# Optimization experiments

Hardware: AMD Instinct MI355X
Metric: run time of the kernel (lower is better)

The kernel has to match this reference:

```python
import jax, jax.numpy as jnp
import numpy as np

EMBED_DIM = 1024
N1 = 4096
N2 = 4096


def setup_inputs() -> dict:
    key = jax.random.key(0)
    ks = jax.random.split(key, 14)
    s = 1.0 / np.sqrt(EMBED_DIM)
    def lin(k):
        kw, kb = jax.random.split(k)
        W = jax.random.uniform(kw, (EMBED_DIM, EMBED_DIM), jnp.float32, -s, s)
        b = jax.random.uniform(kb, (EMBED_DIM,), jnp.float32, -s, s)
        return W, b
    Wq1, bq1 = lin(ks[0]); Wk1, bk1 = lin(ks[1]); Wv1, bv1 = lin(ks[2])
    Wq2, bq2 = lin(ks[3]); Wk2, bk2 = lin(ks[4]); Wv2, bv2 = lin(ks[5])
    x1 = jax.random.normal(ks[6], (N1, EMBED_DIM), jnp.float32)
    x2 = jax.random.normal(ks[7], (N2, EMBED_DIM), jnp.float32)
    return {
        "input_tensor1": x1, "input_tensor2": x2,
        "Wq1": Wq1, "bq1": bq1, "Wk1": Wk1, "bk1": bk1, "Wv1": Wv1, "bv1": bv1,
        "Wq2": Wq2, "bq2": bq2, "Wk2": Wk2, "bk2": bk2, "Wv2": Wv2, "bv2": bv2,
    }


def reference(input_tensor1, input_tensor2,
              Wq1, bq1, Wk1, bk1, Wv1, bv1,
              Wq2, bq2, Wk2, bk2, Wv2, bv2):
    scale = 1.0 / jnp.sqrt(jnp.asarray(EMBED_DIM, input_tensor1.dtype))
    # torch Linear: y = x @ W.T + b
    q1 = input_tensor1 @ Wq1.T + bq1   # [N1, D]
    k1 = input_tensor1 @ Wk1.T + bk1
    v1 = input_tensor1 @ Wv1.T + bv1
    q2 = input_tensor2 @ Wq2.T + bq2   # [N2, D]
    k2 = input_tensor2 @ Wk2.T + bk2
    v2 = input_tensor2 @ Wv2.T + bv2
    # stream-2 queries attend over stream-1 keys/values
    scores1 = (q2 @ k1.T) * scale                  # [N2, N1]
    probs1 = jax.nn.softmax(scores1, axis=-1)      # dropout p=0 -> identity
    context1 = probs1 @ v1                         # [N2, D]
    # stream-1 queries attend over stream-2 keys/values
    scores2 = (q1 @ k2.T) * scale                  # [N1, N2]
    probs2 = jax.nn.softmax(scores2, axis=-1)
    context2 = probs2 @ v2                         # [N1, D]
    return (context1, context2)
```

## Files before the change

kernel.cpp:

```cpp
#include <hip/hip_runtime.h>
#include <hip/hip_bf16.h>
#include <cstdint>
#include <cstddef>

#define DEVINL __device__ __forceinline__

typedef __attribute__((ext_vector_type(4))) float   f32x4;
typedef __bf16 bf16x8 __attribute__((ext_vector_type(8)));
typedef __attribute__((ext_vector_type(4))) short   short4v;
typedef __attribute__((ext_vector_type(4))) float   float4v;

static constexpr int BM = 128, BN = 128, BK = 32;
static constexpr int DIM = 1024;
static constexpr int NTOK = 4096;

DEVINL unsigned short f2bf(float f) {
  unsigned u = __float_as_uint(f);
  u += 0x7FFF + ((u >> 16) & 1);
  return (unsigned short)(u >> 16);
}
DEVINL float bf2f(unsigned short s) {
  return __uint_as_float(((unsigned)s) << 16);
}

DEVINL void gll16(const void* g, void* l) {
  __builtin_amdgcn_global_load_lds(
      (const __attribute__((address_space(1))) void*)g,
      (__attribute__((address_space(3))) void*)l, 16, 0, 0);
}

DEVINL void core256(const unsigned short* __restrict__ A, int lda,
                    const unsigned short* __restrict__ B, int ldb,
                    int K, int brow, int bcol, f32x4 acc[8][4])
{
  __shared__ unsigned short lds[65536];
  const int t = threadIdx.x;
  const int w = t >> 6, l = t & 63;
  const int wr = w >> 2, wc = w & 3;
  const int srow = l >> 3;
  const int scol = ((l & 7) ^ srow) << 3;
  const int l15 = l & 15;
  const int cs0 = (((l >> 4) << 3)      ^ ((l & 7) << 3));
  const int cs1 = ((32 + ((l >> 4) << 3)) ^ ((l & 7) << 3));

  const unsigned short* aL = A + (size_t)(brow * 256 + srow) * lda + scol;
  const unsigned short* bL = B + (size_t)(bcol * 256 + srow) * ldb + scol;

#pragma unroll
  for (int m = 0; m < 8; ++m)
#pragma unroll
    for (int n = 0; n < 4; ++n) {
      f32x4 z = {0.f, 0.f, 0.f, 0.f};
      acc[m][n] = z;
    }

#define STA_(Sbase, h, r, kt)                                                  \
  gll16(aL + (size_t)((r)*128 + (h)*64 + (w << 3)) * lda + (size_t)(kt)*64,    \
        (Sbase) + ((r)*128 + (h)*64 + (w << 3)) * 64)
#define STB_(Sbase, h, r, kt)                                                  \
  { const int g16_ = w + (r)*8;                                                \
    const int r0_ = (g16_ >> 2)*64 + (h)*32 + (g16_ & 3)*8;                    \
    gll16(bL + (size_t)r0_ * ldb + (size_t)(kt)*64, (Sbase) + r0_ * 64); }
#define LDA_(Abase, mh)                                                        \
  _Pragma("unroll")                                                            \
  for (int m4 = 0; m4 < 4; ++m4) {                                             \
    const unsigned short* p_ = (Abase) + (wr*128 + (mh)*64 + m4*16 + l15)*64;  \
    af[m4][0] = *(const bf16x8*)(p_ + cs0);                                    \
    af[m4][1] = *(const bf16x8*)(p_ + cs1);                                    \
  }
#define LDB_(Bbase, nh)                                                        \
  _Pragma("unroll")                                                            \
  for (int n2 = 0; n2 < 2; ++n2) {                                             \
    const unsigned short* p_ = (Bbase) + (wc*64 + (nh)*32 + n2*16 + l15)*64;   \
    bfr[n2][0] = *(const bf16x8*)(p_ + cs0);                                   \
    bfr[n2][1] = *(const bf16x8*)(p_ + cs1);                                   \
  }
#define MF_(mh, nh)                                                            \
  __builtin_amdgcn_s_setprio(1);                                               \
  _Pragma("unroll")                                                            \
  for (int m4 = 0; m4 < 4; ++m4)                                               \
  _Pragma("unroll")                                                            \
  for (int n2 = 0; n2 < 2; ++n2) {                                             \
    f32x4 c_ = acc[(mh)*4 + m4][(nh)*2 + n2];                                  \
    c_ = __builtin_amdgcn_mfma_f32_16x16x32_bf16(af[m4][0], bfr[n2][0], c_, 0,0,0); \
    c_ = __builtin_amdgcn_mfma_f32_16x16x32_bf16(af[m4][1], bfr[n2][1], c_, 0,0,0); \
    acc[(mh)*4 + m4][(nh)*2 + n2] = c_;                                        \
  }                                                                            \
  __builtin_amdgcn_s_setprio(0);
#define VMW4() asm volatile("s_waitcnt vmcnt(4)" ::: "memory")
#define VMW2() asm volatile("s_waitcnt vmcnt(2)" ::: "memory")
#define VMW0() asm volatile("s_waitcnt vmcnt(0)" ::: "memory")
#define LGW()  do { asm volatile("s_waitcnt lgkmcnt(0)" ::: "memory");         \
                    __builtin_amdgcn_sched_barrier(0); } while (0)
#define BARR() do { __builtin_amdgcn_s_barrier();                              \
                    asm volatile("" ::: "memory"); } while (0)

  {
    unsigned short* S0 = lds;
    STA_(S0, 0, 0, 0); STA_(S0, 0, 1, 0);
    STB_(S0 + 16384, 0, 0, 0); STB_(S0 + 16384, 0, 1, 0);
    STA_(S0, 1, 0, 0); STA_(S0, 1, 1, 0);
    STB_(S0 + 16384, 1, 0, 0); STB_(S0 + 16384, 1, 1, 0);
  }

  bf16x8 af[4][2], bfr[2][2];
  const int NT = K >> 6;
  for (int kt = 0; kt < NT - 1; ++kt) {
    const unsigned short* Ab = lds + (kt & 1) * 32768;
    const unsigned short* Bb = Ab + 16384;
    unsigned short* Sa = lds + ((kt & 1) ^ 1) * 32768;
    unsigned short* Sb = Sa + 16384;

    VMW4(); BARR();
    STA_(Sa, 0, 0, kt + 1); STA_(Sa, 0, 1, kt + 1);
    LDA_(Ab, 0); LDB_(Bb, 0);
    LGW(); MF_(0, 0);

    VMW4(); BARR();
    STB_(Sb, 0, 0, kt + 1); STB_(Sb, 0, 1, kt + 1);
    LDA_(Ab, 1);
    LGW(); MF_(1, 0);

    VMW4(); BARR();
    STA_(Sa, 1, 0, kt + 1); STA_(Sa, 1, 1, kt + 1);
    LDB_(Bb, 1);
    LGW(); MF_(1, 1);

    STB_(Sb, 1, 0, kt + 1); STB_(Sb, 1, 1, kt + 1);
    LDA_(Ab, 0);
    LGW(); MF_(0, 1);
  }

  {
    const int kt = NT - 1;
    const unsigned short* Ab = lds + (kt & 1) * 32768;
    const unsigned short* Bb = Ab + 16384;
    VMW4(); BARR();
    LDA_(Ab, 0); LDB_(Bb, 0);
    LGW(); MF_(0, 0);
    VMW2(); BARR();
    LDA_(Ab, 1);
    LGW(); MF_(1, 0);
    VMW0(); BARR();
    LDB_(Bb, 1);
    LGW(); MF_(1, 1);
    LDA_(Ab, 0);
    LGW(); MF_(0, 1);
  }
#undef STA_
#undef STB_
#undef LDA_
#undef LDB_
#undef MF_
#undef VMW4
#undef VMW2
#undef VMW0
#undef LGW
#undef BARR
}

__global__ __launch_bounds__(512, 2)
void gemm256_scores(const unsigned short* __restrict__ A,
                    const unsigned short* __restrict__ B,
                    unsigned short* __restrict__ S, float scale)
{
  f32x4 acc[8][4];
  core256(A, DIM, B, DIM, DIM, blockIdx.y, blockIdx.x, acc);

  const int t = threadIdx.x, w = t >> 6, l = t & 63;
  const int wr = w >> 2, wc = w & 3;
  const int r4 = (l >> 4) * 4, c = l & 15;
  const int row0 = blockIdx.y * 256 + wr * 128;
  const int col0 = blockIdx.x * 256 + wc * 64;
#pragma unroll
  for (int mf = 0; mf < 8; ++mf)
#pragma unroll
    for (int nf = 0; nf < 4; ++nf)
#pragma unroll
      for (int i = 0; i < 4; ++i)
        S[(size_t)(row0 + mf*16 + r4 + i) * NTOK + col0 + nf*16 + c] =
            f2bf(acc[mf][nf][i] * scale);
}

__global__ __launch_bounds__(512, 2)
void qkv256(const unsigned short* __restrict__ x1, const unsigned short* __restrict__ x2,
            const unsigned short* __restrict__ W6,
            const float* bq1, const float* bk1, const float* bv1,
            const float* bq2, const float* bk2, const float* bv2,
            unsigned short* q1, unsigned short* k1, unsigned short* v1T,
            unsigned short* q2, unsigned short* k2, unsigned short* v2T)
{
  const int g = blockIdx.z;
  const unsigned short* A = (g < 3) ? x1 : x2;
  const unsigned short* W = W6 + (size_t)g * (DIM * DIM);
  const float* bias = (g == 0) ? bq1 : (g == 1) ? bk1 : (g == 2) ? bv1
                    : (g == 3) ? bq2 : (g == 4) ? bk2 : bv2;
  unsigned short* out = (g == 0) ? q1 : (g == 1) ? k1 : (g == 2) ? v1T
                      : (g == 3) ? q2 : (g == 4) ? k2 : v2T;
  const bool vT = (g == 2 || g == 5);

  f32x4 acc[8][4];
  core256(A, DIM, W, DIM, DIM, blockIdx.y, blockIdx.x, acc);

  const int t = threadIdx.x, w = t >> 6, l = t & 63;
  const int wr = w >> 2, wc = w & 3;
  const int r4 = (l >> 4) * 4, c = l & 15;
  const int row0 = blockIdx.y * 256 + wr * 128;
  const int col0 = blockIdx.x * 256 + wc * 64;

  float bias_v[4];
#pragma unroll
  for (int nf = 0; nf < 4; ++nf) bias_v[nf] = bias[col0 + nf*16 + c];

  if (!vT) {
#pragma unroll
    for (int mf = 0; mf < 8; ++mf)
#pragma unroll
      for (int nf = 0; nf < 4; ++nf)
#pragma unroll
        for (int i = 0; i < 4; ++i)
          out[(size_t)(row0 + mf*16 + r4 + i) * DIM + col0 + nf*16 + c] =
              f2bf(acc[mf][nf][i] + bias_v[nf]);
  } else {
#pragma unroll
    for (int mf = 0; mf < 8; ++mf)
#pragma unroll
      for (int nf = 0; nf < 4; ++nf) {
        short4v pk;
#pragma unroll
        for (int i = 0; i < 4; ++i) pk[i] = (short)f2bf(acc[mf][nf][i] + bias_v[nf]);
        *(short4v*)(out + (size_t)(col0 + nf*16 + c) * NTOK + row0 + mf*16 + r4) = pk;
      }
  }
}

DEVINL void gemm_core(const unsigned short* __restrict__ A, int lda,
                      const unsigned short* __restrict__ B, int ldb,
                      int kb, int klen, int brow, int bcol,
                      f32x4 acc[4][4], unsigned short* lds)
{
  const int t = threadIdx.x;
  const int wave = t >> 6, lane = t & 63;
  const int wr = wave >> 1, wc = wave & 1;
  const int frow = lane & 15;
  const int kq = (lane >> 4) * 8;
  const int sr = lane >> 2;
  const int sc = (lane & 3) * 8;

  const unsigned short* Arow = A + (size_t)(brow * BM) * lda + kb;
  const unsigned short* Brow = B + (size_t)(bcol * BN) * ldb + kb;

  unsigned short* As0 = lds;
  unsigned short* Bs0 = lds + BM * BK;
  unsigned short* As1 = lds + 2 * BM * BK;
  unsigned short* Bs1 = lds + 3 * BM * BK;

#define STAGE(Asb, Bsb, k0)                                                   \
  {                                                                           \
    _Pragma("unroll")                                                         \
    for (int r = 0; r < 2; ++r) {                                             \
      const int rb = (r * 4 + wave) * 16;                                     \
      gll16(Arow + (size_t)(rb + sr) * lda + (k0) + sc, (Asb) + rb * BK);     \
      gll16(Brow + (size_t)(rb + sr) * ldb + (k0) + sc, (Bsb) + rb * BK);     \
    }                                                                         \
  }

  STAGE(As0, Bs0, 0);
  asm volatile("s_waitcnt vmcnt(0)" ::: "memory");
  __syncthreads();

  const int nt = klen / BK;
  for (int tile = 0; tile < nt; ++tile) {
    unsigned short* Ac = (tile & 1) ? As1 : As0;
    unsigned short* Bc = (tile & 1) ? Bs1 : Bs0;
    unsigned short* An = (tile & 1) ? As0 : As1;
    unsigned short* Bn = (tile & 1) ? Bs0 : Bs1;

    if (tile + 1 < nt) STAGE(An, Bn, (tile + 1) * BK);

    bf16x8 af[4], bfv[4];
#pragma unroll
    for (int m = 0; m < 4; ++m)
      af[m] = *(const bf16x8*)(Ac + (wr * 64 + m * 16 + frow) * BK + kq);
#pragma unroll
    for (int n = 0; n < 4; ++n)
      bfv[n] = *(const bf16x8*)(Bc + (wc * 64 + n * 16 + frow) * BK + kq);

#pragma unroll
    for (int m = 0; m < 4; ++m)
#pragma unroll
      for (int n = 0; n < 4; ++n)
        acc[m][n] = __builtin_amdgcn_mfma_f32_16x16x32_bf16(af[m], bfv[n], acc[m][n], 0, 0, 0);

    asm volatile("s_waitcnt vmcnt(0)" ::: "memory");
    __syncthreads();
  }
#undef STAGE
}

__global__ __launch_bounds__(256, 4)
void gemm_nt_f32(const unsigned short* __restrict__ A, int lda,
                 const unsigned short* __restrict__ B, int ldb,
                 float* __restrict__ Out, float* __restrict__ Part,
                 int klen, int ldo)
{
  __shared__ unsigned short lds[4 * BM * BK];
  f32x4 acc[4][4];
#pragma unroll
  for (int m = 0; m < 4; ++m)
#pragma unroll
    for (int n = 0; n < 4; ++n) {
      f32x4 z = {0.f, 0.f, 0.f, 0.f};
      acc[m][n] = z;
    }
  gemm_core(A, lda, B, ldb, blockIdx.z * klen, klen, blockIdx.y, blockIdx.x, acc, lds);

  float* dst = (blockIdx.z == 0) ? Out : Part;
  const int t = threadIdx.x, wave = t >> 6, lane = t & 63;
  const int wr = wave >> 1, wc = wave & 1;
  const int rr = (lane >> 4) * 4, cc = lane & 15;
#pragma unroll
  for (int m = 0; m < 4; ++m) {
    const int row0 = blockIdx.y * BM + wr * 64 + m * 16 + rr;
#pragma unroll
    for (int n = 0; n < 4; ++n) {
      const int col = blockIdx.x * BN + wc * 64 + n * 16 + cc;
#pragma unroll
      for (int i = 0; i < 4; ++i)
        dst[(size_t)(row0 + i) * ldo + col] = acc[m][n][i];
    }
  }
}

__global__ __launch_bounds__(256)
void add_partial(float* __restrict__ out, const float* __restrict__ part, int n4)
{
  const int i = blockIdx.x * 256 + threadIdx.x;
  if (i < n4) {
    float4v a = ((const float4v*)out)[i];
    float4v b = ((const float4v*)part)[i];
#pragma unroll
    for (int j = 0; j < 4; ++j) a[j] += b[j];
    ((float4v*)out)[i] = a;
  }
}

__global__ __launch_bounds__(256)
void softmax_inplace(unsigned short* __restrict__ S)
{
  const int row = blockIdx.x;
  unsigned short* r = S + (size_t)row * NTOK;
  const int t = threadIdx.x, wave = t >> 6, lane = t & 63;
  __shared__ float red[4];

  bf16x8 d0 = *(const bf16x8*)(r + t * 8);
  bf16x8 d1 = *(const bf16x8*)(r + 2048 + t * 8);
  float v[16];
  {
    const unsigned short* p0 = (const unsigned short*)&d0;
    const unsigned short* p1 = (const unsigned short*)&d1;
#pragma unroll
    for (int j = 0; j < 8; ++j) { v[j] = bf2f(p0[j]); v[8 + j] = bf2f(p1[j]); }
  }
  float mx = v[0];
#pragma unroll
  for (int j = 1; j < 16; ++j) mx = fmaxf(mx, v[j]);
#pragma unroll
  for (int o = 32; o > 0; o >>= 1) mx = fmaxf(mx, __shfl_xor(mx, o));
  if (lane == 0) red[wave] = mx;
  __syncthreads();
  mx = fmaxf(fmaxf(red[0], red[1]), fmaxf(red[2], red[3]));

  float s = 0.f;
#pragma unroll
  for (int j = 0; j < 16; ++j) { v[j] = __expf(v[j] - mx); s += v[j]; }
#pragma unroll
  for (int o = 32; o > 0; o >>= 1) s += __shfl_xor(s, o);
  __syncthreads();
  if (lane == 0) red[wave] = s;
  __syncthreads();
  s = red[0] + red[1] + red[2] + red[3];
  const float inv = 1.0f / s;

  unsigned short o0[8], o1[8];
#pragma unroll
  for (int j = 0; j < 8; ++j) { o0[j] = f2bf(v[j] * inv); o1[j] = f2bf(v[8 + j] * inv); }
  *(bf16x8*)(r + t * 8)        = *(const bf16x8*)o0;
  *(bf16x8*)(r + 2048 + t * 8) = *(const bf16x8*)o1;
}

__global__ __launch_bounds__(256)
void cvt2(const float* __restrict__ a, const float* __restrict__ b,
          unsigned short* __restrict__ oa, unsigned short* __restrict__ ob)
{
  const float* in = blockIdx.y ? b : a;
  unsigned short* out = blockIdx.y ? ob : oa;
  const size_t i = ((size_t)blockIdx.x * 256 + threadIdx.x) * 4;
  float4v x = *(const float4v*)(in + i);
  short4v o;
#pragma unroll
  for (int j = 0; j < 4; ++j) o[j] = (short)f2bf(x[j]);
  *(short4v*)(out + i) = o;
}

__global__ __launch_bounds__(256)
void cvt_w(const float* w0, const float* w1, const float* w2,
           const float* w3, const float* w4, const float* w5,
           unsigned short* __restrict__ W6)
{
  const float* srcs[6] = {w0, w1, w2, w3, w4, w5};
  const float* in = srcs[blockIdx.y];
  unsigned short* out = W6 + (size_t)blockIdx.y * (DIM * DIM);
  const size_t i = ((size_t)blockIdx.x * 256 + threadIdx.x) * 4;
  float4v x = *(const float4v*)(in + i);
  short4v o;
#pragma unroll
  for (int j = 0; j < 4; ++j) o[j] = (short)f2bf(x[j]);
  *(short4v*)(out + i) = o;
}

extern "C" void kernel_launch(void* const* d_in, const int* in_sizes, int n_in,
                              void* d_out, int out_size, void* d_ws, size_t ws_size,
                              hipStream_t stream)
{
  const float* x1  = (const float*)d_in[0];
  const float* x2  = (const float*)d_in[1];
  const float* Wq1 = (const float*)d_in[2];  const float* bq1 = (const float*)d_in[3];
  const float* Wk1 = (const float*)d_in[4];  const float* bk1 = (const float*)d_in[5];
  const float* Wv1 = (const float*)d_in[6];  const float* bv1 = (const float*)d_in[7];
  const float* Wq2 = (const float*)d_in[8];  const float* bq2 = (const float*)d_in[9];
  const float* Wk2 = (const float*)d_in[10]; const float* bk2 = (const float*)d_in[11];
  const float* Wv2 = (const float*)d_in[12]; const float* bv2 = (const float*)d_in[13];
  float* out = (float*)d_out;

  unsigned short* ws  = (unsigned short*)d_ws;
  const size_t NTD = (size_t)NTOK * DIM;
  unsigned short* x1b = ws;
  unsigned short* x2b = x1b + NTD;
  unsigned short* W6  = x2b + NTD;
  unsigned short* q1  = W6 + 6 * (size_t)(DIM * DIM);
  unsigned short* k1  = q1 + NTD;
  unsigned short* v1T = k1 + NTD;
  unsigned short* q2  = v1T + NTD;
  unsigned short* k2  = q2 + NTD;
  unsigned short* v2T = k2 + NTD;
  unsigned short* S   = v2T + NTD;
  float* P1 = (float*)ws;

  const dim3 blk(256);
  cvt2 <<<dim3(NTD / 1024, 2), blk, 0, stream>>>(x1, x2, x1b, x2b);
  cvt_w<<<dim3((DIM * DIM) / 1024, 6), blk, 0, stream>>>(Wq1, Wk1, Wv1, Wq2, Wk2, Wv2, W6);

  qkv256<<<dim3(DIM / 256, NTOK / 256, 6), dim3(512), 0, stream>>>(
      x1b, x2b, W6, bq1, bk1, bv1, bq2, bk2, bv2, q1, k1, v1T, q2, k2, v2T);

  const float scale = 0.03125f;
  const int KH = NTOK / 2;

  gemm256_scores<<<dim3(NTOK / 256, NTOK / 256), dim3(512), 0, stream>>>(q2, k1, S, scale);
  softmax_inplace<<<dim3(NTOK), blk, 0, stream>>>(S);
  gemm_nt_f32<<<dim3(DIM / BN, NTOK / BM, 2), blk, 0, stream>>>(S, NTOK, v1T, NTOK, out, P1, KH, DIM);
  add_partial<<<dim3((NTD / 4 + 255) / 256), blk, 0, stream>>>(out, P1, NTD / 4);

  gemm256_scores<<<dim3(NTOK / 256, NTOK / 256), dim3(512), 0, stream>>>(q1, k2, S, scale);
  softmax_inplace<<<dim3(NTOK), blk, 0, stream>>>(S);
  gemm_nt_f32<<<dim3(DIM / BN, NTOK / BM, 2), blk, 0, stream>>>(S, NTOK, v2T, NTOK, out + NTD, P1, KH, DIM);
  add_partial<<<dim3((NTD / 4 + 255) / 256), blk, 0, stream>>>(out + NTD, P1, NTD / 4);
}
```

Before: 287.9 us.

## Fuse both PV GEMMs into one 256-tile launch and regroup core256 prefetch stages

Both probability-times-V products now run in a single launch that reuses the 256x256 core256 tile with 512 threads, replacing the two smaller 128x128 gemm_nt_f32 calls. The K dimension is split in two along grid z, followed by a single add pass over both outputs. The workspace is re-laid out so both score matrices live side by side, overwriting the freed x/W buffers, and the two V^T buffers are contiguous. The core256 mainloop now issues the A and B prefetches for each half together and drops one barrier per iteration. The aim is fewer launches and less per-iteration sync. The cost is a different wait/overlap pattern, plus workspace aliasing that has to be correct.

```diff
diff --git a/kernel.cpp b/kernel.cpp
--- a/kernel.cpp
+++ b/kernel.cpp
@@ -10,7 +10,6 @@
 typedef __attribute__((ext_vector_type(4))) short   short4v;
 typedef __attribute__((ext_vector_type(4))) float   float4v;
 
-static constexpr int BM = 128, BN = 128, BK = 32;
 static constexpr int DIM = 1024;
 static constexpr int NTOK = 4096;
 
@@ -40,7 +39,7 @@
   const int srow = l >> 3;
   const int scol = ((l & 7) ^ srow) << 3;
   const int l15 = l & 15;
-  const int cs0 = (((l >> 4) << 3)      ^ ((l & 7) << 3));
+  const int cs0 = (((l >> 4) << 3)       ^ ((l & 7) << 3));
   const int cs1 = ((32 + ((l >> 4) << 3)) ^ ((l & 7) << 3));
 
   const unsigned short* aL = A + (size_t)(brow * 256 + srow) * lda + scol;
@@ -88,7 +87,6 @@
   }                                                                            \
   __builtin_amdgcn_s_setprio(0);
 #define VMW4() asm volatile("s_waitcnt vmcnt(4)" ::: "memory")
-#define VMW2() asm volatile("s_waitcnt vmcnt(2)" ::: "memory")
 #define VMW0() asm volatile("s_waitcnt vmcnt(0)" ::: "memory")
 #define LGW()  do { asm volatile("s_waitcnt lgkmcnt(0)" ::: "memory");         \
                     __builtin_amdgcn_sched_barrier(0); } while (0)
@@ -96,11 +94,10 @@
                     asm volatile("" ::: "memory"); } while (0)
 
   {
-    unsigned short* S0 = lds;
-    STA_(S0, 0, 0, 0); STA_(S0, 0, 1, 0);
-    STB_(S0 + 16384, 0, 0, 0); STB_(S0 + 16384, 0, 1, 0);
-    STA_(S0, 1, 0, 0); STA_(S0, 1, 1, 0);
-    STB_(S0 + 16384, 1, 0, 0); STB_(S0 + 16384, 1, 1, 0);
+    unsigned short* S0  = lds;
+    unsigned short* S0b = lds + 16384;
+    STA_(S0, 0, 0, 0); STA_(S0, 0, 1, 0); STB_(S0b, 0, 0, 0); STB_(S0b, 0, 1, 0);
+    STA_(S0, 1, 0, 0); STA_(S0, 1, 1, 0); STB_(S0b, 1, 0, 0); STB_(S0b, 1, 1, 0);
   }
 
   bf16x8 af[4][2], bfr[2][2];
@@ -113,20 +110,19 @@
 
     VMW4(); BARR();
     STA_(Sa, 0, 0, kt + 1); STA_(Sa, 0, 1, kt + 1);
+    STB_(Sb, 0, 0, kt + 1); STB_(Sb, 0, 1, kt + 1);
     LDA_(Ab, 0); LDB_(Bb, 0);
     LGW(); MF_(0, 0);
 
     VMW4(); BARR();
-    STB_(Sb, 0, 0, kt + 1); STB_(Sb, 0, 1, kt + 1);
+    STA_(Sa, 1, 0, kt + 1); STA_(Sa, 1, 1, kt + 1);
+    STB_(Sb, 1, 0, kt + 1); STB_(Sb, 1, 1, kt + 1);
     LDA_(Ab, 1);
     LGW(); MF_(1, 0);
 
-    VMW4(); BARR();
-    STA_(Sa, 1, 0, kt + 1); STA_(Sa, 1, 1, kt + 1);
     LDB_(Bb, 1);
     LGW(); MF_(1, 1);
 
-    STB_(Sb, 1, 0, kt + 1); STB_(Sb, 1, 1, kt + 1);
     LDA_(Ab, 0);
     LGW(); MF_(0, 1);
   }
@@ -138,10 +134,9 @@
     VMW4(); BARR();
     LDA_(Ab, 0); LDB_(Bb, 0);
     LGW(); MF_(0, 0);
-    VMW2(); BARR();
+    VMW0(); BARR();
     LDA_(Ab, 1);
     LGW(); MF_(1, 0);
-    VMW0(); BARR();
     LDB_(Bb, 1);
     LGW(); MF_(1, 1);
     LDA_(Ab, 0);
@@ -153,7 +148,6 @@
 #undef LDB_
 #undef MF_
 #undef VMW4
-#undef VMW2
 #undef VMW0
 #undef LGW
 #undef BARR
@@ -234,115 +228,56 @@
   }
 }
 
-DEVINL void gemm_core(const unsigned short* __restrict__ A, int lda,
-                      const unsigned short* __restrict__ B, int ldb,
-                      int kb, int klen, int brow, int bcol,
-                      f32x4 acc[4][4], unsigned short* lds)
-{
-  const int t = threadIdx.x;
-  const int wave = t >> 6, lane = t & 63;
-  const int wr = wave >> 1, wc = wave & 1;
-  const int frow = lane & 15;
-  const int kq = (lane >> 4) * 8;
-  const int sr = lane >> 2;
-  const int sc = (lane & 3) * 8;
-
-  const unsigned short* Arow = A + (size_t)(brow * BM) * lda + kb;
-  const unsigned short* Brow = B + (size_t)(bcol * BN) * ldb + kb;
-
-  unsigned short* As0 = lds;
-  unsigned short* Bs0 = lds + BM * BK;
-  unsigned short* As1 = lds + 2 * BM * BK;
-  unsigned short* Bs1 = lds + 3 * BM * BK;
-
-#define STAGE(Asb, Bsb, k0)                                                   \
-  {                                                                           \
-    _Pragma("unroll")                                                         \
-    for (int r = 0; r < 2; ++r) {                                             \
-      const int rb = (r * 4 + wave) * 16;                                     \
-      gll16(Arow + (size_t)(rb + sr) * lda + (k0) + sc, (Asb) + rb * BK);     \
-      gll16(Brow + (size_t)(rb + sr) * ldb + (k0) + sc, (Bsb) + rb * BK);     \
-    }                                                                         \
-  }
-
-  STAGE(As0, Bs0, 0);
-  asm volatile("s_waitcnt vmcnt(0)" ::: "memory");
-  __syncthreads();
-
-  const int nt = klen / BK;
-  for (int tile = 0; tile < nt; ++tile) {
-    unsigned short* Ac = (tile & 1) ? As1 : As0;
-    unsigned short* Bc = (tile & 1) ? Bs1 : Bs0;
-    unsigned short* An = (tile & 1) ? As0 : As1;
-    unsigned short* Bn = (tile & 1) ? Bs0 : Bs1;
-
-    if (tile + 1 < nt) STAGE(An, Bn, (tile + 1) * BK);
-
-    bf16x8 af[4], bfv[4];
-#pragma unroll
-    for (int m = 0; m < 4; ++m)
-      af[m] = *(const bf16x8*)(Ac + (wr * 64 + m * 16 + frow) * BK + kq);
-#pragma unroll
-    for (int n = 0; n < 4; ++n)
-      bfv[n] = *(const bf16x8*)(Bc + (wc * 64 + n * 16 + frow) * BK + kq);
-
-#pragma unroll
-    for (int m = 0; m < 4; ++m)
-#pragma unroll
-      for (int n = 0; n < 4; ++n)
-        acc[m][n] = __builtin_amdgcn_mfma_f32_16x16x32_bf16(af[m], bfv[n], acc[m][n], 0, 0, 0);
-
-    asm volatile("s_waitcnt vmcnt(0)" ::: "memory");
-    __syncthreads();
-  }
-#undef STAGE
-}
-
-__global__ __launch_bounds__(256, 4)
-void gemm_nt_f32(const unsigned short* __restrict__ A, int lda,
-                 const unsigned short* __restrict__ B, int ldb,
-                 float* __restrict__ Out, float* __restrict__ Part,
-                 int klen, int ldo)
-{
-  __shared__ unsigned short lds[4 * BM * BK];
-  f32x4 acc[4][4];
-#pragma unroll
-  for (int m = 0; m < 4; ++m)
-#pragma unroll
-    for (int n = 0; n < 4; ++n) {
-      f32x4 z = {0.f, 0.f, 0.f, 0.f};
-      acc[m][n] = z;
-    }
-  gemm_core(A, lda, B, ldb, blockIdx.z * klen, klen, blockIdx.y, blockIdx.x, acc, lds);
-
-  float* dst = (blockIdx.z == 0) ? Out : Part;
-  const int t = threadIdx.x, wave = t >> 6, lane = t & 63;
-  const int wr = wave >> 1, wc = wave & 1;
-  const int rr = (lane >> 4) * 4, cc = lane & 15;
-#pragma unroll
-  for (int m = 0; m < 4; ++m) {
-    const int row0 = blockIdx.y * BM + wr * 64 + m * 16 + rr;
-#pragma unroll
-    for (int n = 0; n < 4; ++n) {
-      const int col = blockIdx.x * BN + wc * 64 + n * 16 + cc;
-#pragma unroll
-      for (int i = 0; i < 4; ++i)
-        dst[(size_t)(row0 + i) * ldo + col] = acc[m][n][i];
-    }
-  }
+__global__ __launch_bounds__(512, 2)
+void pv_fused(const unsigned short* __restrict__ S1,
+              const unsigned short* __restrict__ S2,
+              const unsigned short* __restrict__ vTcat,
+              float* __restrict__ out, float* __restrict__ P)
+{
+  const int bx = blockIdx.x, by = blockIdx.y, z = blockIdx.z;
+  const unsigned short* A = ((bx < 4) ? S1 : S2) + (size_t)z * 2048;
+  const unsigned short* B = vTcat + (size_t)z * 2048;
+
+  f32x4 acc[8][4];
+  core256(A, NTOK, B, NTOK, 2048, by, bx, acc);
+
+  const int t = threadIdx.x, w = t >> 6, l = t & 63;
+  const int wr = w >> 2, wc = w & 3;
+  const int r4 = (l >> 4) * 4, c = l & 15;
+  const int row0 = by * 256 + wr * 128;
+  const int col0 = bx * 256 + wc * 64;
+
+#pragma unroll
+  for (int mf = 0; mf < 8; ++mf)
+#pragma unroll
+    for (int nf = 0; nf < 4; ++nf)
+#pragma unroll
+      for (int i = 0; i < 4; ++i) {
+        const int r = row0 + mf*16 + r4 + i;
+        const int cg = col0 + nf*16 + c;
+        if (z) {
+          P[(size_t)r * 2048 + cg] = acc[mf][nf][i];
+        } else {
+          float* dst = (cg < 1024) ? (out + (size_t)r * 1024 + cg)
+                                   : (out + 4194304 + (size_t)r * 1024 + (cg - 1024));
+          *dst = acc[mf][nf][i];
+        }
+      }
 }
 
 __global__ __launch_bounds__(256)
-void add_partial(float* __restrict__ out, const float* __restrict__ part, int n4)
-{
-  const int i = blockIdx.x * 256 + threadIdx.x;
-  if (i < n4) {
-    float4v a = ((const float4v*)out)[i];
-    float4v b = ((const float4v*)part)[i];
-#pragma unroll
-    for (int j = 0; j < 4; ++j) a[j] += b[j];
-    ((float4v*)out)[i] = a;
-  }
+void add_pv(float* __restrict__ out, const float* __restrict__ P)
+{
+  const int idx = blockIdx.x * 256 + threadIdx.x;
+  const int r  = idx >> 9;
+  const int c4 = (idx & 511) << 2;
+  const float4v p = *(const float4v*)(P + (size_t)r * 2048 + c4);
+  float* dst = (c4 < 1024) ? (out + (size_t)r * 1024 + c4)
+                           : (out + 4194304 + (size_t)r * 1024 + (c4 - 1024));
+  float4v a = *(const float4v*)dst;
+#pragma unroll
+  for (int j = 0; j < 4; ++j) a[j] += p[j];
+  *(float4v*)dst = a;
 }
 
 __global__ __launch_bounds__(256)
@@ -435,17 +370,20 @@
 
   unsigned short* ws  = (unsigned short*)d_ws;
   const size_t NTD = (size_t)NTOK * DIM;
+  const size_t SM  = (size_t)NTOK * NTOK;
   unsigned short* x1b = ws;
   unsigned short* x2b = x1b + NTD;
   unsigned short* W6  = x2b + NTD;
-  unsigned short* q1  = W6 + 6 * (size_t)(DIM * DIM);
+  unsigned short* S1  = ws;
+  unsigned short* S2  = ws + SM;
+  unsigned short* q1  = ws + 2 * SM;
   unsigned short* k1  = q1 + NTD;
-  unsigned short* v1T = k1 + NTD;
-  unsigned short* q2  = v1T + NTD;
+  unsigned short* q2  = k1 + NTD;
   unsigned short* k2  = q2 + NTD;
-  unsigned short* v2T = k2 + NTD;
-  unsigned short* S   = v2T + NTD;
-  float* P1 = (float*)ws;
+  unsigned short* vT  = k2 + NTD;
+  unsigned short* v1T = vT;
+  unsigned short* v2T = vT + NTD;
+  float* P = (float*)q1;
 
   const dim3 blk(256);
   cvt2 <<<dim3(NTD / 1024, 2), blk, 0, stream>>>(x1, x2, x1b, x2b);
@@ -455,15 +393,12 @@
       x1b, x2b, W6, bq1, bk1, bv1, bq2, bk2, bv2, q1, k1, v1T, q2, k2, v2T);
 
   const float scale = 0.03125f;
-  const int KH = NTOK / 2;
-
-  gemm256_scores<<<dim3(NTOK / 256, NTOK / 256), dim3(512), 0, stream>>>(q2, k1, S, scale);
-  softmax_inplace<<<dim3(NTOK), blk, 0, stream>>>(S);
-  gemm_nt_f32<<<dim3(DIM / BN, NTOK / BM, 2), blk, 0, stream>>>(S, NTOK, v1T, NTOK, out, P1, KH, DIM);
-  add_partial<<<dim3((NTD / 4 + 255) / 256), blk, 0, stream>>>(out, P1, NTD / 4);
-
-  gemm256_scores<<<dim3(NTOK / 256, NTOK / 256), dim3(512), 0, stream>>>(q1, k2, S, scale);
-  softmax_inplace<<<dim3(NTOK), blk, 0, stream>>>(S);
-  gemm_nt_f32<<<dim3(DIM / BN, NTOK / BM, 2), blk, 0, stream>>>(S, NTOK, v2T, NTOK, out + NTD, P1, KH, DIM);
-  add_partial<<<dim3((NTD / 4 + 255) / 256), blk, 0, stream>>>(out + NTD, P1, NTD / 4);
-}
+
+  gemm256_scores<<<dim3(NTOK / 256, NTOK / 256), dim3(512), 0, stream>>>(q2, k1, S1, scale);
+  softmax_inplace<<<dim3(NTOK), blk, 0, stream>>>(S1);
+  gemm256_scores<<<dim3(NTOK / 256, NTOK / 256), dim3(512), 0, stream>>>(q1, k2, S2, scale);
+  softmax_inplace<<<dim3(NTOK), blk, 0, stream>>>(S2);
+
+  pv_fused<<<dim3(8, NTOK / 256, 2), dim3(512), 0, stream>>>(S1, S2, vT, out, P);
+  add_pv<<<dim3(8192), blk, 0, stream>>>(out, P);
+}
```

New measurement: 261.0 us. 1.1x faster.
